# Kernel optimization log

Hardware: AMD Instinct MI355X
Metric: run time of the kernel (lower is better)

The kernel has to match this reference:

```python
import jax, jax.numpy as jnp
import numpy as np

B, S, D = 1024, 60, 256   # seq_len=60 is hard-coded by nn.Linear(dim*60, n_experts)
H = 1024                  # d_inner
E = 8                     # n_experts
TOPK = 2
CAP = B * TOPK // E       # balanced per-expert capacity = 256


def setup_inputs() -> dict:
    key = jax.random.key(0)
    ks = jax.random.split(key, 9)
    s = 0.02
    return {
        "x":        jax.random.normal(ks[0], (B, S, D), dtype=jnp.float32),
        "W_switch": jax.random.normal(ks[1], (S * D, E), dtype=jnp.float32) * s,
        "b_switch": jnp.zeros((E,), dtype=jnp.float32),
        "W1":       jax.random.normal(ks[2], (E, D, H), dtype=jnp.float32) * s,
        "b1":       jnp.zeros((E, H), dtype=jnp.float32),
        "W2":       jax.random.normal(ks[3], (E, H, D), dtype=jnp.float32) * s,
        "b2":       jnp.zeros((E, D), dtype=jnp.float32),
        "gamma":    jnp.ones((D,), dtype=jnp.float32),
        "beta":     jnp.zeros((D,), dtype=jnp.float32),
    }


def reference(x, W_switch, b_switch, W1, b1, W2, b2, gamma, beta):
    # --- routing: softmax over experts per batch element ---
    logits = x.reshape(B, S * D) @ W_switch + b_switch          # [B, E]
    probs = jax.nn.softmax(logits, axis=-1)
    # balanced dispatch: each expert takes its top-CAP batch indices
    _, idx = jax.lax.top_k(probs.T, CAP)                        # [E, CAP] int32
    xe = x[idx]                                                 # gather -> [E, CAP, S, D]
    # --- per-expert grouped GEMMs (Column- then Row-parallel linear) ---
    h = jax.nn.gelu(jnp.einsum('ecsd,edh->ecsh', xe, W1)
                    + b1[:, None, None, :], approximate=False)  # [E, CAP, S, H]
    oe = jnp.einsum('ecsh,ehd->ecsd', h, W2) + b2[:, None, None, :]  # [E, CAP, S, D]
    # --- scatter-combine via index_add over the batch dim ---
    out = jnp.zeros_like(x).at[idx.reshape(-1)].add(oe.reshape(E * CAP, S, D))
    # --- residual + post-LayerNorm (pre_lnorm=False) ---
    z = x + out
    mu = jnp.mean(z, axis=-1, keepdims=True)
    var = jnp.var(z, axis=-1, keepdims=True)
    return (z - mu) * jax.lax.rsqrt(var + 1e-5) * gamma + beta
```

## Files before the change

### kernel.cpp

```cpp
#include <hip/hip_runtime.h>
#include <hip/hip_bf16.h>
#include <math.h>

#define NB   1024
#define NS   60
#define ND   256
#define NH   1024
#define NE   8
#define NCAP 256
#define NTOK (NCAP*NS)
#define BM   64
#define NBLK (NTOK/BM)

typedef __attribute__((ext_vector_type(8)))  short short8;
typedef __attribute__((ext_vector_type(16))) float floatx16;

__device__ __forceinline__ unsigned short f2bf(float f) {
    union { float f; unsigned u; } cv; cv.f = f;
    unsigned u = cv.u;
    u += 0x7FFFu + ((u >> 16) & 1u);
    return (unsigned short)(u >> 16);
}
__device__ __forceinline__ float bf2f(unsigned short h) {
    union { unsigned u; float f; } c; c.u = ((unsigned)h) << 16; return c.f;
}
__device__ __forceinline__ unsigned cvt_pk_bf16(float a, float b) {
#if defined(__has_builtin) && __has_builtin(__builtin_amdgcn_cvt_pk_bf16_f32)
    typedef __attribute__((ext_vector_type(2))) __bf16 bf16x2;
    union { bf16x2 v; unsigned u; } cc;
    cc.v = __builtin_amdgcn_cvt_pk_bf16_f32(a, b);
    return cc.u;
#else
    return (unsigned)f2bf(a) | ((unsigned)f2bf(b) << 16);
#endif
}

#define GELU_H0  0.39894228f
#define GELU_H1 -0.065680755f
#define GELU_H2  0.008727065f
#define GELU_H3 -0.000664585f
#define GELU_H4  2.07274e-5f
__device__ __forceinline__ float fast_gelu(float xx) {
    float t = __builtin_amdgcn_fmed3f(xx, -3.25f, 3.25f);
    float s = t * t;
    float p = fmaf(s, GELU_H4, GELU_H3);
    p = fmaf(s, p, GELU_H2);
    p = fmaf(s, p, GELU_H1);
    p = fmaf(s, p, GELU_H0);
    return xx * fmaf(t, p, 0.5f);
}

__global__ __launch_bounds__(256)
void k_route_pack(const float* __restrict__ x, const float* __restrict__ Wsw,
                  unsigned short* __restrict__ xb, float* __restrict__ partials,
                  int* __restrict__ cntb,
                  const float* __restrict__ W1, const float* __restrict__ W2,
                  unsigned short* __restrict__ W1t, unsigned short* __restrict__ W2t) {
    if (blockIdx.x >= 1024) {
        int idx = (blockIdx.x - 1024) * 256 + threadIdx.x;
        int lane = idx & 63;
        int m31 = lane & 31, hi = lane >> 5;
        const float* src;
        unsigned short* dst;
        int ldk;
        if (idx < 262144) {
            int fi = idx >> 6;
            int kt = fi & 15;
            int ht = (fi >> 4) & 31;
            int e  = fi >> 9;
            int k0 = kt * 16 + hi * 8;
            int h  = ht * 32 + m31;
            src = W1 + ((size_t)(e * 256 + k0)) * 1024 + h;
            dst = W1t + (size_t)fi * 512 + lane * 8;
            ldk = 1024;
        } else {
            int i2 = idx - 262144;
            int fi = i2 >> 6;
            int kt = fi & 63;
            int dt = (fi >> 6) & 7;
            int e  = fi >> 9;
            int k0 = kt * 16 + hi * 8;
            int d  = dt * 32 + m31;
            src = W2 + ((size_t)(e * 1024 + k0)) * 256 + d;
            dst = W2t + (size_t)fi * 512 + lane * 8;
            ldk = 256;
        }
        float v[8];
#pragma unroll
        for (int j = 0; j < 8; ++j) v[j] = src[(size_t)j * ldk];
        uint4 o;
        o.x = cvt_pk_bf16(v[0], v[1]);
        o.y = cvt_pk_bf16(v[2], v[3]);
        o.z = cvt_pk_bf16(v[4], v[5]);
        o.w = cvt_pk_bf16(v[6], v[7]);
        *(uint4*)dst = o;
        return;
    }
    if (blockIdx.x < 4) cntb[blockIdx.x * 256 + threadIdx.x] = 0;
    int g = blockIdx.x & 127;
    int s = blockIdx.x >> 7;
    int team = threadIdx.x >> 5;
    int j = threadIdx.x & 31;
    int b = g * 8 + team;
    const float* xr = x + (size_t)b * 15360 + s * 1920;
    unsigned short* xbr = xb + (size_t)b * 15360 + s * 1920;
    float a[8];
#pragma unroll
    for (int e = 0; e < 8; ++e) a[e] = 0.f;
    for (int it = 0; it < 15; ++it) {
        int k = it * 128 + j * 4;
        float4 xv = *(const float4*)(xr + k);
        uint2 pk = {cvt_pk_bf16(xv.x, xv.y), cvt_pk_bf16(xv.z, xv.w)};
        *(uint2*)(xbr + k) = pk;
        float xa[4] = {xv.x, xv.y, xv.z, xv.w};
        const float* w = Wsw + (size_t)(s * 1920 + k) * 8;
#pragma unroll
        for (int c = 0; c < 4; ++c) {
            float4 w0 = *(const float4*)(w + c * 8);
            float4 w1 = *(const float4*)(w + c * 8 + 4);
            float xc = xa[c];
            a[0] += xc * w0.x; a[1] += xc * w0.y; a[2] += xc * w0.z; a[3] += xc * w0.w;
            a[4] += xc * w1.x; a[5] += xc * w1.y; a[6] += xc * w1.z; a[7] += xc * w1.w;
        }
    }
#pragma unroll
    for (int m = 16; m >= 1; m >>= 1) {
#pragma unroll
        for (int e = 0; e < 8; ++e) a[e] += __shfl_xor(a[e], m);
    }
    if (j == 0) {
        float4* p = (float4*)(partials + ((size_t)(s * 1024) + b) * 8);
        p[0] = make_float4(a[0], a[1], a[2], a[3]);
        p[1] = make_float4(a[4], a[5], a[6], a[7]);
    }
}

__global__ __launch_bounds__(256)
void k_topk(const float* __restrict__ partials, const float* __restrict__ bsw,
            int* __restrict__ idxb, int* __restrict__ cntb, int* __restrict__ slotb) {
    __shared__ float v[NB];
    int e = blockIdx.x >> 2;
    int q = blockIdx.x & 3;
    int tid = threadIdx.x;
    float bs[8];
#pragma unroll
    for (int i = 0; i < 8; ++i) bs[i] = bsw[i];
#pragma unroll
    for (int rr = 0; rr < 4; ++rr) {
        int row = rr * 256 + tid;
        float l[8];
#pragma unroll
        for (int i = 0; i < 8; ++i) l[i] = bs[i];
#pragma unroll
        for (int s = 0; s < 8; ++s) {
            const float4* p = (const float4*)(partials + ((size_t)(s * 1024) + row) * 8);
            float4 p0 = p[0], p1 = p[1];
            l[0] += p0.x; l[1] += p0.y; l[2] += p0.z; l[3] += p0.w;
            l[4] += p1.x; l[5] += p1.y; l[6] += p1.z; l[7] += p1.w;
        }
        float m = l[0];
#pragma unroll
        for (int i = 1; i < 8; ++i) m = fmaxf(m, l[i]);
        float sum = 0.f;
#pragma unroll
        for (int i = 0; i < 8; ++i) sum += expf(l[i] - m);
        v[row] = expf(l[e] - m) / sum;
    }
    __syncthreads();
    int cand = q * 256 + tid;
    float mv = v[cand];
    int cnt = 0;
    for (int jj = 0; jj < NB; ++jj) {
        float vj = v[jj];
        cnt += (vj > mv) || (vj == mv && jj < cand);
    }
    if (cnt < NCAP) {
        idxb[e * NCAP + cnt] = cand;
        int pos = atomicAdd(&cntb[cand], 1);
        slotb[cand * 8 + pos] = e * NCAP + cnt;
    }
}

__global__ __launch_bounds__(256, 3)
void k_mlp(const unsigned short* __restrict__ xb,
           const unsigned short* __restrict__ W1t,
           const unsigned short* __restrict__ W2t,
           const float* __restrict__ b1,
           const float* __restrict__ b2,
           const int* __restrict__ idxb,
           unsigned short* __restrict__ oe) {
    __shared__ __align__(16) unsigned short Xf[16384];
    __shared__ __align__(16) unsigned short Pf[8192];

    int e  = blockIdx.x & 7;
    int bm = blockIdx.x >> 3;
    int tb = bm * BM;
    int tid = threadIdx.x;
    int lane = tid & 63, w = tid >> 6;
    int m31 = lane & 31, hi = lane >> 5;
    const short8* xfrag = (const short8*)Xf;
    const short8* pfrag = (const short8*)Pf;

    {
        int lr = tid >> 2;
        int s4 = tid & 3;
        int t = tb + lr;
        int c = t / 60;
        int s = t - c * 60;
        int bidx = idxb[e * NCAP + c];
        const unsigned short* src = xb + ((size_t)(bidx * 60 + s)) * 256;
        int nt = lr >> 5, mm = lr & 31;
#pragma unroll
        for (int jj = 0; jj < 8; ++jj) {
            int u = jj * 4 + s4;
            int kt = u >> 1, uh = u & 1;
            *(short8*)(&Xf[(((nt * 16 + kt) * 64) + uh * 32 + mm) * 8]) =
                *(const short8*)(src + u * 8);
        }
    }
    __syncthreads();

    floatx16 acc2[2][2];
#pragma unroll
    for (int mt = 0; mt < 2; ++mt)
#pragma unroll
        for (int nt = 0; nt < 2; ++nt) acc2[mt][nt] = 0.f;

    for (int ch = 0; ch < 8; ++ch) {
        floatx16 pacc[2];
        pacc[0] = 0.f; pacc[1] = 0.f;
        int ht = ch * 4 + w;
        const unsigned short* w1p = W1t + ((size_t)(e * 32 + ht) * 16) * 512 + lane * 8;
        __builtin_amdgcn_s_setprio(1);
#pragma unroll 4
        for (int kt = 0; kt < 16; ++kt) {
            short8 aw = *(const short8*)(w1p + (size_t)kt * 512);
            short8 bx0 = xfrag[kt * 64 + lane];
            short8 bx1 = xfrag[(16 + kt) * 64 + lane];
            pacc[0] = __builtin_amdgcn_mfma_f32_32x32x16_bf16(aw, bx0, pacc[0], 0, 0, 0);
            pacc[1] = __builtin_amdgcn_mfma_f32_32x32x16_bf16(aw, bx1, pacc[1], 0, 0, 0);
        }
        __builtin_amdgcn_s_setprio(0);
        __syncthreads();
        const float* b1c = b1 + e * NH + ch * 128 + w * 32;
#pragma unroll
        for (int q = 0; q < 4; ++q) {
            float4 bb = *(const float4*)(b1c + 8 * q + 4 * hi);
            float bv[4] = {bb.x, bb.y, bb.z, bb.w};
            int ktp = w * 2 + (q >> 1);
#pragma unroll
            for (int nt = 0; nt < 2; ++nt) {
                float g[4];
#pragma unroll
                for (int r = 0; r < 4; ++r)
                    g[r] = fast_gelu(pacc[nt][4 * q + r] + bv[r]);
                uint2 pk = {cvt_pk_bf16(g[0], g[1]), cvt_pk_bf16(g[2], g[3])};
                *(uint2*)(&Pf[(((nt * 8 + ktp) * 64) + (q & 1) * 32 + m31) * 8 + 4 * hi]) = pk;
            }
        }
        __syncthreads();
        __builtin_amdgcn_s_setprio(1);
#pragma unroll 4
        for (int kt = 0; kt < 8; ++kt) {
            short8 bp0 = pfrag[kt * 64 + lane];
            short8 bp1 = pfrag[(8 + kt) * 64 + lane];
#pragma unroll
            for (int mt = 0; mt < 2; ++mt) {
                short8 aw = *(const short8*)(W2t +
                    ((size_t)((e * 8 + w * 2 + mt) * 64 + ch * 8 + kt)) * 512 + lane * 8);
                acc2[mt][0] = __builtin_amdgcn_mfma_f32_32x32x16_bf16(aw, bp0, acc2[mt][0], 0, 0, 0);
                acc2[mt][1] = __builtin_amdgcn_mfma_f32_32x32x16_bf16(aw, bp1, acc2[mt][1], 0, 0, 0);
            }
        }
        __builtin_amdgcn_s_setprio(0);
    }

#pragma unroll
    for (int mt = 0; mt < 2; ++mt) {
#pragma unroll
        for (int q = 0; q < 4; ++q) {
            int dd = w * 64 + mt * 32 + 8 * q + 4 * hi;
            float4 bb = *(const float4*)(b2 + e * ND + dd);
            float bv[4] = {bb.x, bb.y, bb.z, bb.w};
            int u16 = dd >> 3;
#pragma unroll
            for (int nt = 0; nt < 2; ++nt) {
                int row = nt * 32 + m31;
                int up = u16 ^ (row & 15);
                uint2 pk = {cvt_pk_bf16(acc2[mt][nt][4 * q + 0] + bv[0],
                                        acc2[mt][nt][4 * q + 1] + bv[1]),
                            cvt_pk_bf16(acc2[mt][nt][4 * q + 2] + bv[2],
                                        acc2[mt][nt][4 * q + 3] + bv[3])};
                *(uint2*)(&Xf[row * 256 + up * 8 + 4 * hi]) = pk;
            }
        }
    }
    __syncthreads();
    {
        int row = tid >> 2;
        int c = tid & 3;
        unsigned short* dst = oe + ((size_t)(e * NTOK + tb + row)) * 256;
#pragma unroll
        for (int uu = 0; uu < 8; ++uu) {
            int u = c + uu * 4;
            int up = u ^ (row & 15);
            *(short8*)(dst + u * 8) = *(const short8*)(&Xf[row * 256 + up * 8]);
        }
    }
}

__global__ void k_ln(const float* __restrict__ x, const unsigned short* __restrict__ oe,
                     const int* __restrict__ cntb, const int* __restrict__ slotb,
                     const float* __restrict__ gamma, const float* __restrict__ beta,
                     float* __restrict__ out) {
    int row = blockIdx.x * 4 + (threadIdx.x >> 6);
    int lane = threadIdx.x & 63;
    int b = row / 60;
    int s = row - b * 60;
    float4 v = ((const float4*)(x + (size_t)row * 256))[lane];
    int cnt = cntb[b];
    const int* sl = slotb + b * 8;
    for (int i = 0; i < cnt; ++i) {
        int slot = sl[i];
        ushort4 ov = ((const ushort4*)(oe + ((size_t)slot * 60 + s) * 256))[lane];
        v.x += bf2f(ov.x); v.y += bf2f(ov.y); v.z += bf2f(ov.z); v.w += bf2f(ov.w);
    }
    float sm = v.x + v.y + v.z + v.w;
    float q = v.x * v.x + v.y * v.y + v.z * v.z + v.w * v.w;
#pragma unroll
    for (int off = 32; off >= 1; off >>= 1) {
        sm += __shfl_xor(sm, off);
        q  += __shfl_xor(q, off);
    }
    float mu  = sm * (1.0f / 256.0f);
    float var = q * (1.0f / 256.0f) - mu * mu;
    float rs  = rsqrtf(var + 1e-5f);
    float4 g  = ((const float4*)gamma)[lane];
    float4 bt = ((const float4*)beta)[lane];
    float4 o;
    o.x = (v.x - mu) * rs * g.x + bt.x;
    o.y = (v.y - mu) * rs * g.y + bt.y;
    o.z = (v.z - mu) * rs * g.z + bt.z;
    o.w = (v.w - mu) * rs * g.w + bt.w;
    ((float4*)(out + (size_t)row * 256))[lane] = o;
}

extern "C" void kernel_launch(void* const* d_in, const int* in_sizes, int n_in,
                              void* d_out, int out_size, void* d_ws, size_t ws_size,
                              hipStream_t stream) {
    const float* x     = (const float*)d_in[0];
    const float* Wsw   = (const float*)d_in[1];
    const float* bsw   = (const float*)d_in[2];
    const float* W1    = (const float*)d_in[3];
    const float* b1    = (const float*)d_in[4];
    const float* W2    = (const float*)d_in[5];
    const float* b2    = (const float*)d_in[6];
    const float* gamma = (const float*)d_in[7];
    const float* beta  = (const float*)d_in[8];
    float* out = (float*)d_out;

    char* ws = (char*)d_ws;
    size_t off = 0;
    auto alloc = [&](size_t bytes) { void* p = ws + off; off += (bytes + 255) & ~255ull; return p; };
    float*          partials = (float*)alloc((size_t)8 * NB * NE * 4);
    int*            idxb     = (int*)alloc((size_t)NE * NCAP * 4);
    int*            cntb     = (int*)alloc((size_t)NB * 4);
    int*            slotb    = (int*)alloc((size_t)NB * 8 * 4);
    unsigned short* xb       = (unsigned short*)alloc((size_t)NB * NS * ND * 2);
    unsigned short* W1t      = (unsigned short*)alloc((size_t)NE * ND * NH * 2);
    unsigned short* W2t      = (unsigned short*)alloc((size_t)NE * NH * ND * 2);
    unsigned short* oe       = (unsigned short*)alloc((size_t)NE * NTOK * ND * 2);
    (void)ws_size; (void)in_sizes; (void)n_in; (void)out_size;

    k_route_pack<<<3072, 256, 0, stream>>>(x, Wsw, xb, partials, cntb, W1, W2, W1t, W2t);
    k_topk<<<32, 256, 0, stream>>>(partials, bsw, idxb, cntb, slotb);
    k_mlp<<<NE * NBLK, 256, 0, stream>>>(xb, W1t, W2t, b1, b2, idxb, oe);
    k_ln<<<NB * NS / 4, 256, 0, stream>>>(x, oe, cntb, slotb, gamma, beta, out);
}
```

Before: 393.0 us.

## Split k_mlp work across eight waves per block instead of four

The fused MLP kernel now launches 512 threads per block. Each of the 8 waves computes a single 32x32 tile of the first GEMM (one hidden slice and one token half) and one 32-row slice of the output in the second GEMM, where before each of 4 waves handled two tiles in each stage. This halves per-wave accumulator registers and raises the number of waves per CU, which should hide memory latency better. The s_setprio hints are removed. In exchange, each wave has less independent MFMA work to overlap, and the first GEMM reloads each W1 fragment in two waves.

```diff
diff --git a/kernel.cpp b/kernel.cpp
--- a/kernel.cpp
+++ b/kernel.cpp
@@ -181,7 +181,7 @@
     }
 }
 
-__global__ __launch_bounds__(256, 3)
+__global__ __launch_bounds__(512, 4)
 void k_mlp(const unsigned short* __restrict__ xb,
            const unsigned short* __restrict__ W1t,
            const unsigned short* __restrict__ W2t,
@@ -196,14 +196,15 @@
     int bm = blockIdx.x >> 3;
     int tb = bm * BM;
     int tid = threadIdx.x;
-    int lane = tid & 63, w = tid >> 6;
+    int lane = tid & 63, wv = tid >> 6;
     int m31 = lane & 31, hi = lane >> 5;
+    int ht = wv & 3, nt1 = wv >> 2;
     const short8* xfrag = (const short8*)Xf;
     const short8* pfrag = (const short8*)Pf;
 
     {
-        int lr = tid >> 2;
-        int s4 = tid & 3;
+        int lr = tid >> 3;
+        int s8 = tid & 7;
         int t = tb + lr;
         int c = t / 60;
         int s = t - c * 60;
@@ -211,8 +212,8 @@
         const unsigned short* src = xb + ((size_t)(bidx * 60 + s)) * 256;
         int nt = lr >> 5, mm = lr & 31;
 #pragma unroll
-        for (int jj = 0; jj < 8; ++jj) {
-            int u = jj * 4 + s4;
+        for (int jj = 0; jj < 4; ++jj) {
+            int u = jj * 8 + s8;
             int kt = u >> 1, uh = u & 1;
             *(short8*)(&Xf[(((nt * 16 + kt) * 64) + uh * 32 + mm) * 8]) =
                 *(const short8*)(src + u * 8);
@@ -220,89 +221,72 @@
     }
     __syncthreads();
 
-    floatx16 acc2[2][2];
-#pragma unroll
-    for (int mt = 0; mt < 2; ++mt)
-#pragma unroll
-        for (int nt = 0; nt < 2; ++nt) acc2[mt][nt] = 0.f;
+    floatx16 acc2[2];
+    acc2[0] = 0.f; acc2[1] = 0.f;
 
     for (int ch = 0; ch < 8; ++ch) {
-        floatx16 pacc[2];
-        pacc[0] = 0.f; pacc[1] = 0.f;
-        int ht = ch * 4 + w;
-        const unsigned short* w1p = W1t + ((size_t)(e * 32 + ht) * 16) * 512 + lane * 8;
-        __builtin_amdgcn_s_setprio(1);
+        floatx16 pacc;
+        pacc = 0.f;
+        const unsigned short* w1p =
+            W1t + ((size_t)(e * 32 + ch * 4 + ht) * 16) * 512 + lane * 8;
 #pragma unroll 4
         for (int kt = 0; kt < 16; ++kt) {
             short8 aw = *(const short8*)(w1p + (size_t)kt * 512);
-            short8 bx0 = xfrag[kt * 64 + lane];
-            short8 bx1 = xfrag[(16 + kt) * 64 + lane];
-            pacc[0] = __builtin_amdgcn_mfma_f32_32x32x16_bf16(aw, bx0, pacc[0], 0, 0, 0);
-            pacc[1] = __builtin_amdgcn_mfma_f32_32x32x16_bf16(aw, bx1, pacc[1], 0, 0, 0);
-        }
-        __builtin_amdgcn_s_setprio(0);
+            short8 bx = xfrag[(nt1 * 16 + kt) * 64 + lane];
+            pacc = __builtin_amdgcn_mfma_f32_32x32x16_bf16(aw, bx, pacc, 0, 0, 0);
+        }
         __syncthreads();
-        const float* b1c = b1 + e * NH + ch * 128 + w * 32;
+        const float* b1c = b1 + e * NH + ch * 128 + ht * 32;
 #pragma unroll
         for (int q = 0; q < 4; ++q) {
             float4 bb = *(const float4*)(b1c + 8 * q + 4 * hi);
             float bv[4] = {bb.x, bb.y, bb.z, bb.w};
-            int ktp = w * 2 + (q >> 1);
-#pragma unroll
-            for (int nt = 0; nt < 2; ++nt) {
-                float g[4];
-#pragma unroll
-                for (int r = 0; r < 4; ++r)
-                    g[r] = fast_gelu(pacc[nt][4 * q + r] + bv[r]);
-                uint2 pk = {cvt_pk_bf16(g[0], g[1]), cvt_pk_bf16(g[2], g[3])};
-                *(uint2*)(&Pf[(((nt * 8 + ktp) * 64) + (q & 1) * 32 + m31) * 8 + 4 * hi]) = pk;
-            }
+            int ktp = ht * 2 + (q >> 1);
+            float g[4];
+#pragma unroll
+            for (int r = 0; r < 4; ++r)
+                g[r] = fast_gelu(pacc[4 * q + r] + bv[r]);
+            uint2 pk = {cvt_pk_bf16(g[0], g[1]), cvt_pk_bf16(g[2], g[3])};
+            *(uint2*)(&Pf[(((nt1 * 8 + ktp) * 64) + (q & 1) * 32 + m31) * 8 + 4 * hi]) = pk;
         }
         __syncthreads();
-        __builtin_amdgcn_s_setprio(1);
+        const unsigned short* w2p =
+            W2t + ((size_t)((e * 8 + wv) * 64 + ch * 8)) * 512 + lane * 8;
 #pragma unroll 4
         for (int kt = 0; kt < 8; ++kt) {
             short8 bp0 = pfrag[kt * 64 + lane];
             short8 bp1 = pfrag[(8 + kt) * 64 + lane];
-#pragma unroll
-            for (int mt = 0; mt < 2; ++mt) {
-                short8 aw = *(const short8*)(W2t +
-                    ((size_t)((e * 8 + w * 2 + mt) * 64 + ch * 8 + kt)) * 512 + lane * 8);
-                acc2[mt][0] = __builtin_amdgcn_mfma_f32_32x32x16_bf16(aw, bp0, acc2[mt][0], 0, 0, 0);
-                acc2[mt][1] = __builtin_amdgcn_mfma_f32_32x32x16_bf16(aw, bp1, acc2[mt][1], 0, 0, 0);
-            }
-        }
-        __builtin_amdgcn_s_setprio(0);
-    }
-
-#pragma unroll
-    for (int mt = 0; mt < 2; ++mt) {
-#pragma unroll
-        for (int q = 0; q < 4; ++q) {
-            int dd = w * 64 + mt * 32 + 8 * q + 4 * hi;
-            float4 bb = *(const float4*)(b2 + e * ND + dd);
-            float bv[4] = {bb.x, bb.y, bb.z, bb.w};
-            int u16 = dd >> 3;
-#pragma unroll
-            for (int nt = 0; nt < 2; ++nt) {
-                int row = nt * 32 + m31;
-                int up = u16 ^ (row & 15);
-                uint2 pk = {cvt_pk_bf16(acc2[mt][nt][4 * q + 0] + bv[0],
-                                        acc2[mt][nt][4 * q + 1] + bv[1]),
-                            cvt_pk_bf16(acc2[mt][nt][4 * q + 2] + bv[2],
-                                        acc2[mt][nt][4 * q + 3] + bv[3])};
-                *(uint2*)(&Xf[row * 256 + up * 8 + 4 * hi]) = pk;
-            }
+            short8 aw = *(const short8*)(w2p + (size_t)kt * 512);
+            acc2[0] = __builtin_amdgcn_mfma_f32_32x32x16_bf16(aw, bp0, acc2[0], 0, 0, 0);
+            acc2[1] = __builtin_amdgcn_mfma_f32_32x32x16_bf16(aw, bp1, acc2[1], 0, 0, 0);
+        }
+    }
+
+#pragma unroll
+    for (int q = 0; q < 4; ++q) {
+        int dd = wv * 32 + 8 * q + 4 * hi;
+        float4 bb = *(const float4*)(b2 + e * ND + dd);
+        float bv[4] = {bb.x, bb.y, bb.z, bb.w};
+        int u16 = 4 * wv + q;
+#pragma unroll
+        for (int nt = 0; nt < 2; ++nt) {
+            int row = nt * 32 + m31;
+            int up = u16 ^ (row & 15);
+            uint2 pk = {cvt_pk_bf16(acc2[nt][4 * q + 0] + bv[0],
+                                    acc2[nt][4 * q + 1] + bv[1]),
+                        cvt_pk_bf16(acc2[nt][4 * q + 2] + bv[2],
+                                    acc2[nt][4 * q + 3] + bv[3])};
+            *(uint2*)(&Xf[row * 256 + up * 8 + 4 * hi]) = pk;
         }
     }
     __syncthreads();
     {
-        int row = tid >> 2;
-        int c = tid & 3;
+        int row = tid >> 3;
+        int c = tid & 7;
         unsigned short* dst = oe + ((size_t)(e * NTOK + tb + row)) * 256;
 #pragma unroll
-        for (int uu = 0; uu < 8; ++uu) {
-            int u = c + uu * 4;
+        for (int uu = 0; uu < 4; ++uu) {
+            int u = c + uu * 8;
             int up = u ^ (row & 15);
             *(short8*)(dst + u * 8) = *(const short8*)(&Xf[row * 256 + up * 8]);
         }
@@ -374,6 +358,6 @@
 
     k_route_pack<<<3072, 256, 0, stream>>>(x, Wsw, xb, partials, cntb, W1, W2, W1t, W2t);
     k_topk<<<32, 256, 0, stream>>>(partials, bsw, idxb, cntb, slotb);
-    k_mlp<<<NE * NBLK, 256, 0, stream>>>(xb, W1t, W2t, b1, b2, idxb, oe);
+    k_mlp<<<NE * NBLK, 512, 0, stream>>>(xb, W1t, W2t, b1, b2, idxb, oe);
     k_ln<<<NB * NS / 4, 256, 0, stream>>>(x, oe, cntb, slotb, gamma, beta, out);
 }
```

Result: no change. 395.8 us (+0.7%).
